# Optimization experiments

Measured on AMD Instinct MI355X. Metric: run time of the kernel, lower is better.

Reference implementation:

```python
import jax, jax.numpy as jnp
import numpy as np

EPS = 1e-05


def _inv_sqrt_22(M):
    # M: [C, 2, 2] SPD. Closed-form sqrt via trace/det, then analytic 2x2 inverse.
    a, b = M[:, 0, 0], M[:, 0, 1]
    c, d = M[:, 1, 0], M[:, 1, 1]
    s = jnp.sqrt(a * d - b * c)            # sqrt(det)
    t = jnp.sqrt(a + d + 2.0 * s)          # sqrt(trace + 2*sqrt(det))
    # M_sqrt = (M + s*I)/t ; invert analytically
    sa, sb, sc, sd = (a + s) / t, b / t, c / t, (d + s) / t
    det_sqrt = sa * sd - sb * sc
    inv = jnp.stack([jnp.stack([sd, -sb], -1), jnp.stack([-sc, sa], -1)], -2)
    return inv / det_sqrt[:, None, None]   # [C, 2, 2]


def setup_inputs() -> dict:
    key = jax.random.key(0)
    k1, k2, k3 = jax.random.split(key, 3)
    B, C, H, W = 32, 64, 128, 128
    z = jax.random.normal(k1, (B, C, H, W, 2), dtype=jnp.float32)
    gamma = jax.random.normal(k2, (2, 2), dtype=jnp.float32)
    beta = jax.random.normal(k3, (2,), dtype=jnp.float32)
    return {"z": z, "gamma": gamma, "beta": beta}


def reference(z, gamma, beta):
    # z: [B, C, H, W, 2] real view of a complex feature map (training-mode path)
    B, C, H, W, _ = z.shape
    mu = jnp.mean(z, axis=(0, 2, 3), keepdims=True)          # [1,C,1,1,2]
    xc = z - mu
    # per-channel 2x2 covariance
    sigma = jnp.einsum('bchwi,bchwj->cij', xc, xc) / (B * H * W)
    sigma = sigma + EPS * jnp.eye(2, dtype=z.dtype)
    w = _inv_sqrt_22(sigma)                                   # [C,2,2]
    o = jnp.einsum('cij,bchwj->bchwi', w, xc)                 # whiten
    o = jnp.einsum('ij,bchwj->bchwi', gamma, o) + beta        # affine
    return o
```

## Files before the change

kernel.cpp:

```cpp
#include <hip/hip_runtime.h>
#include <math.h>

#define EPS 1e-5

constexpr int B = 32, C = 64, H = 128, W = 128;
constexpr int HW = H * W;
constexpr int NSAMP = B * HW;
constexpr int PLANE_FLOATS = HW * 2;
constexpr int PLANE_F4 = PLANE_FLOATS / 4;
constexpr int PLANES = B * C;

typedef float vfloat4 __attribute__((ext_vector_type(4)));

__global__ __launch_bounds__(256) void reduce_kernel(const float* __restrict__ z,
                                                     float* __restrict__ ws) {
    const int blk = blockIdx.x;
    const vfloat4* p = (const vfloat4*)(z + (size_t)blk * PLANE_FLOATS);

    float s0 = 0.f, s1 = 0.f, s00 = 0.f, s01 = 0.f, s11 = 0.f;
    for (int base = 0; base < PLANE_F4; base += 1024) {
        const int i = base + threadIdx.x;
        vfloat4 v0 = p[i];
        vfloat4 v1 = p[i + 256];
        vfloat4 v2 = p[i + 512];
        vfloat4 v3 = p[i + 768];
        s0  += (v0.x + v0.z) + (v1.x + v1.z) + (v2.x + v2.z) + (v3.x + v3.z);
        s1  += (v0.y + v0.w) + (v1.y + v1.w) + (v2.y + v2.w) + (v3.y + v3.w);
        s00 += (v0.x * v0.x + v0.z * v0.z) + (v1.x * v1.x + v1.z * v1.z)
             + (v2.x * v2.x + v2.z * v2.z) + (v3.x * v3.x + v3.z * v3.z);
        s11 += (v0.y * v0.y + v0.w * v0.w) + (v1.y * v1.y + v1.w * v1.w)
             + (v2.y * v2.y + v2.w * v2.w) + (v3.y * v3.y + v3.w * v3.w);
        s01 += (v0.x * v0.y + v0.z * v0.w) + (v1.x * v1.y + v1.z * v1.w)
             + (v2.x * v2.y + v2.z * v2.w) + (v3.x * v3.y + v3.z * v3.w);
    }

    #pragma unroll
    for (int o = 32; o > 0; o >>= 1) {
        s0  += __shfl_down(s0,  o, 64);
        s1  += __shfl_down(s1,  o, 64);
        s00 += __shfl_down(s00, o, 64);
        s01 += __shfl_down(s01, o, 64);
        s11 += __shfl_down(s11, o, 64);
    }

    __shared__ float sm[5][4];
    const int lane = threadIdx.x & 63;
    const int wv = threadIdx.x >> 6;
    if (lane == 0) {
        sm[0][wv] = s0; sm[1][wv] = s1; sm[2][wv] = s00; sm[3][wv] = s01; sm[4][wv] = s11;
    }
    __syncthreads();
    if (threadIdx.x == 0) {
        float t0 = 0.f, t1 = 0.f, t2 = 0.f, t3 = 0.f, t4 = 0.f;
        #pragma unroll
        for (int w = 0; w < 4; w++) {
            t0 += sm[0][w]; t1 += sm[1][w]; t2 += sm[2][w]; t3 += sm[3][w]; t4 += sm[4][w];
        }
        float* wp = ws + (size_t)blk * 8;
        wp[0] = t0; wp[1] = t1; wp[2] = t2; wp[3] = t3; wp[4] = t4;
    }
}

__global__ __launch_bounds__(256) void apply_kernel(const float* __restrict__ z,
                                                    const float* __restrict__ ws,
                                                    const float* __restrict__ gamma,
                                                    const float* __restrict__ beta,
                                                    float* __restrict__ out) {
    const int blk = blockIdx.x;
    const int c = blk & (C - 1);

    __shared__ float tr[6];
    if (threadIdx.x < 64) {
        float a0 = 0.f, a1 = 0.f, a2 = 0.f, a3 = 0.f, a4 = 0.f;
        if (threadIdx.x < B) {
            const float* wp = ws + (size_t)(threadIdx.x * C + c) * 8;
            a0 = wp[0]; a1 = wp[1]; a2 = wp[2]; a3 = wp[3]; a4 = wp[4];
        }
        #pragma unroll
        for (int o = 16; o > 0; o >>= 1) {
            a0 += __shfl_down(a0, o, 64);
            a1 += __shfl_down(a1, o, 64);
            a2 += __shfl_down(a2, o, 64);
            a3 += __shfl_down(a3, o, 64);
            a4 += __shfl_down(a4, o, 64);
        }
        if (threadIdx.x == 0) {
            const double S0 = a0, S1 = a1, S00 = a2, S01 = a3, S11 = a4;
            const double invN = 1.0 / (double)NSAMP;
            const double mu0 = S0 * invN, mu1 = S1 * invN;
            const double va = S00 * invN - mu0 * mu0 + EPS;
            const double vb = S01 * invN - mu0 * mu1;
            const double vd = S11 * invN - mu1 * mu1 + EPS;
            const double sdet = sqrt(va * vd - vb * vb);
            const double tt = sqrt(va + vd + 2.0 * sdet);
            const double sa = (va + sdet) / tt;
            const double sb = vb / tt;
            const double sd2 = (vd + sdet) / tt;
            const double inv_det = 1.0 / (sa * sd2 - sb * sb);
            const double w00 =  sd2 * inv_det;
            const double w01 = -sb  * inv_det;
            const double w11 =  sa  * inv_det;
            const double g00 = gamma[0], g01 = gamma[1], g10 = gamma[2], g11 = gamma[3];
            const double A00 = g00 * w00 + g01 * w01;
            const double A01 = g00 * w01 + g01 * w11;
            const double A10 = g10 * w00 + g11 * w01;
            const double A11 = g10 * w01 + g11 * w11;
            tr[0] = (float)A00; tr[1] = (float)A01; tr[2] = (float)A10; tr[3] = (float)A11;
            tr[4] = (float)((double)beta[0] - (A00 * mu0 + A01 * mu1));
            tr[5] = (float)((double)beta[1] - (A10 * mu0 + A11 * mu1));
        }
    }
    __syncthreads();
    const float A00 = tr[0], A01 = tr[1], A10 = tr[2], A11 = tr[3];
    const float b0 = tr[4], b1 = tr[5];

    const vfloat4* p = (const vfloat4*)(z + (size_t)blk * PLANE_FLOATS);
    vfloat4* q = (vfloat4*)(out + (size_t)blk * PLANE_FLOATS);
    for (int base = PLANE_F4 - 1024; base >= 0; base -= 1024) {
        const int i = base + threadIdx.x;
        vfloat4 v0 = p[i];
        vfloat4 v1 = p[i + 256];
        vfloat4 v2 = p[i + 512];
        vfloat4 v3 = p[i + 768];
        vfloat4 r0, r1, r2, r3;
        r0.x = A00 * v0.x + A01 * v0.y + b0;  r0.y = A10 * v0.x + A11 * v0.y + b1;
        r0.z = A00 * v0.z + A01 * v0.w + b0;  r0.w = A10 * v0.z + A11 * v0.w + b1;
        r1.x = A00 * v1.x + A01 * v1.y + b0;  r1.y = A10 * v1.x + A11 * v1.y + b1;
        r1.z = A00 * v1.z + A01 * v1.w + b0;  r1.w = A10 * v1.z + A11 * v1.w + b1;
        r2.x = A00 * v2.x + A01 * v2.y + b0;  r2.y = A10 * v2.x + A11 * v2.y + b1;
        r2.z = A00 * v2.z + A01 * v2.w + b0;  r2.w = A10 * v2.z + A11 * v2.w + b1;
        r3.x = A00 * v3.x + A01 * v3.y + b0;  r3.y = A10 * v3.x + A11 * v3.y + b1;
        r3.z = A00 * v3.z + A01 * v3.w + b0;  r3.w = A10 * v3.z + A11 * v3.w + b1;
        __builtin_nontemporal_store(r0, &q[i]);
        __builtin_nontemporal_store(r1, &q[i + 256]);
        __builtin_nontemporal_store(r2, &q[i + 512]);
        __builtin_nontemporal_store(r3, &q[i + 768]);
    }
}

extern "C" void kernel_launch(void* const* d_in, const int* in_sizes, int n_in,
                              void* d_out, int out_size, void* d_ws, size_t ws_size,
                              hipStream_t stream) {
    (void)in_sizes; (void)n_in; (void)out_size; (void)ws_size;
    const float* z     = (const float*)d_in[0];
    const float* gamma = (const float*)d_in[1];
    const float* beta  = (const float*)d_in[2];
    float* out = (float*)d_out;
    float* ws  = (float*)d_ws;

    reduce_kernel<<<PLANES, 256, 0, stream>>>(z, ws);
    apply_kernel<<<PLANES, 256, 0, stream>>>(z, ws, gamma, beta, out);
}
```

Baseline: 476.8 us.

## Fuse reduce and apply into one persistent kernel with per-channel flag sync

Replaces the two-kernel reduce/apply scheme with one kernel of 256 blocks of 1024 threads, each owning a quarter of the batch for one channel. Blocks publish partial sums, bump a per-channel atomic counter and spin until all four quarters arrive, then build the affine transform and apply it, re-reading their planes in reverse order to hit in cache. The aim is to remove one launch and reuse cached input between the reduce and apply phases. The risks are a deadlock if the blocks are not all co-resident, lower parallelism from fewer blocks, and an extra memset launch.

```diff
diff --git a/kernel.cpp b/kernel.cpp
--- a/kernel.cpp
+++ b/kernel.cpp
@@ -8,30 +8,50 @@
 constexpr int NSAMP = B * HW;
 constexpr int PLANE_FLOATS = HW * 2;
 constexpr int PLANE_F4 = PLANE_FLOATS / 4;
-constexpr int PLANES = B * C;
+constexpr int QUARTERS = 4;
+constexpr int PLANES_PER_BLK = B / QUARTERS;
+constexpr int NBLOCKS = C * QUARTERS;
+constexpr int NTHREADS = 1024;
 
 typedef float vfloat4 __attribute__((ext_vector_type(4)));
 
-__global__ __launch_bounds__(256) void reduce_kernel(const float* __restrict__ z,
-                                                     float* __restrict__ ws) {
-    const int blk = blockIdx.x;
-    const vfloat4* p = (const vfloat4*)(z + (size_t)blk * PLANE_FLOATS);
+__device__ __forceinline__ float agent_load_f32(const float* a) {
+    unsigned int u = __hip_atomic_load((const unsigned int*)a,
+                                       __ATOMIC_RELAXED, __HIP_MEMORY_SCOPE_AGENT);
+    return __uint_as_float(u);
+}
+
+__global__ __launch_bounds__(NTHREADS) void fused_kernel(
+    const float* __restrict__ z, float* __restrict__ ws,
+    const float* __restrict__ gamma, const float* __restrict__ beta,
+    float* __restrict__ out)
+{
+    const int k = blockIdx.x;
+    const int c = k & (C - 1);
+    const int q = k >> 6;
+    int* flags = (int*)ws;
+    float* part = ws + 64;
 
     float s0 = 0.f, s1 = 0.f, s00 = 0.f, s01 = 0.f, s11 = 0.f;
-    for (int base = 0; base < PLANE_F4; base += 1024) {
-        const int i = base + threadIdx.x;
-        vfloat4 v0 = p[i];
-        vfloat4 v1 = p[i + 256];
-        vfloat4 v2 = p[i + 512];
-        vfloat4 v3 = p[i + 768];
-        s0  += (v0.x + v0.z) + (v1.x + v1.z) + (v2.x + v2.z) + (v3.x + v3.z);
-        s1  += (v0.y + v0.w) + (v1.y + v1.w) + (v2.y + v2.w) + (v3.y + v3.w);
-        s00 += (v0.x * v0.x + v0.z * v0.z) + (v1.x * v1.x + v1.z * v1.z)
-             + (v2.x * v2.x + v2.z * v2.z) + (v3.x * v3.x + v3.z * v3.z);
-        s11 += (v0.y * v0.y + v0.w * v0.w) + (v1.y * v1.y + v1.w * v1.w)
-             + (v2.y * v2.y + v2.w * v2.w) + (v3.y * v3.y + v3.w * v3.w);
-        s01 += (v0.x * v0.y + v0.z * v0.w) + (v1.x * v1.y + v1.z * v1.w)
-             + (v2.x * v2.y + v2.z * v2.w) + (v3.x * v3.y + v3.z * v3.w);
+    for (int j = 0; j < PLANES_PER_BLK; ++j) {
+        const int plane = (q * PLANES_PER_BLK + j) * C + c;
+        const vfloat4* p = (const vfloat4*)(z + (size_t)plane * PLANE_FLOATS);
+        #pragma unroll
+        for (int base = 0; base < PLANE_F4; base += 4096) {
+            const int i = base + threadIdx.x;
+            vfloat4 v0 = p[i];
+            vfloat4 v1 = p[i + 1024];
+            vfloat4 v2 = p[i + 2048];
+            vfloat4 v3 = p[i + 3072];
+            s0  += (v0.x + v0.z) + (v1.x + v1.z) + (v2.x + v2.z) + (v3.x + v3.z);
+            s1  += (v0.y + v0.w) + (v1.y + v1.w) + (v2.y + v2.w) + (v3.y + v3.w);
+            s00 += (v0.x * v0.x + v0.z * v0.z) + (v1.x * v1.x + v1.z * v1.z)
+                 + (v2.x * v2.x + v2.z * v2.z) + (v3.x * v3.x + v3.z * v3.z);
+            s11 += (v0.y * v0.y + v0.w * v0.w) + (v1.y * v1.y + v1.w * v1.w)
+                 + (v2.y * v2.y + v2.w * v2.w) + (v3.y * v3.y + v3.w * v3.w);
+            s01 += (v0.x * v0.y + v0.z * v0.w) + (v1.x * v1.y + v1.z * v1.w)
+                 + (v2.x * v2.y + v2.z * v2.w) + (v3.x * v3.y + v3.z * v3.w);
+        }
     }
 
     #pragma unroll
@@ -43,98 +63,94 @@
         s11 += __shfl_down(s11, o, 64);
     }
 
-    __shared__ float sm[5][4];
+    __shared__ float sm[5][16];
     const int lane = threadIdx.x & 63;
     const int wv = threadIdx.x >> 6;
     if (lane == 0) {
         sm[0][wv] = s0; sm[1][wv] = s1; sm[2][wv] = s00; sm[3][wv] = s01; sm[4][wv] = s11;
     }
     __syncthreads();
+
+    __shared__ float tr[6];
     if (threadIdx.x == 0) {
         float t0 = 0.f, t1 = 0.f, t2 = 0.f, t3 = 0.f, t4 = 0.f;
         #pragma unroll
-        for (int w = 0; w < 4; w++) {
+        for (int w = 0; w < 16; w++) {
             t0 += sm[0][w]; t1 += sm[1][w]; t2 += sm[2][w]; t3 += sm[3][w]; t4 += sm[4][w];
         }
-        float* wp = ws + (size_t)blk * 8;
+        float* wp = part + (size_t)k * 8;
         wp[0] = t0; wp[1] = t1; wp[2] = t2; wp[3] = t3; wp[4] = t4;
-    }
-}
+        __threadfence();
+        atomicAdd(&flags[c], 1);
 
-__global__ __launch_bounds__(256) void apply_kernel(const float* __restrict__ z,
-                                                    const float* __restrict__ ws,
-                                                    const float* __restrict__ gamma,
-                                                    const float* __restrict__ beta,
-                                                    float* __restrict__ out) {
-    const int blk = blockIdx.x;
-    const int c = blk & (C - 1);
+        while (__hip_atomic_load(&flags[c], __ATOMIC_ACQUIRE,
+                                 __HIP_MEMORY_SCOPE_AGENT) < QUARTERS) {
+            __builtin_amdgcn_s_sleep(8);
+        }
 
-    __shared__ float tr[6];
-    if (threadIdx.x < 64) {
-        float a0 = 0.f, a1 = 0.f, a2 = 0.f, a3 = 0.f, a4 = 0.f;
-        if (threadIdx.x < B) {
-            const float* wp = ws + (size_t)(threadIdx.x * C + c) * 8;
-            a0 = wp[0]; a1 = wp[1]; a2 = wp[2]; a3 = wp[3]; a4 = wp[4];
+        double S0 = 0.0, S1 = 0.0, S00 = 0.0, S01 = 0.0, S11 = 0.0;
+        #pragma unroll
+        for (int qq = 0; qq < QUARTERS; ++qq) {
+            const float* pp = part + (size_t)(qq * C + c) * 8;
+            S0  += (double)agent_load_f32(pp + 0);
+            S1  += (double)agent_load_f32(pp + 1);
+            S00 += (double)agent_load_f32(pp + 2);
+            S01 += (double)agent_load_f32(pp + 3);
+            S11 += (double)agent_load_f32(pp + 4);
         }
-        #pragma unroll
-        for (int o = 16; o > 0; o >>= 1) {
-            a0 += __shfl_down(a0, o, 64);
-            a1 += __shfl_down(a1, o, 64);
-            a2 += __shfl_down(a2, o, 64);
-            a3 += __shfl_down(a3, o, 64);
-            a4 += __shfl_down(a4, o, 64);
-        }
-        if (threadIdx.x == 0) {
-            const double S0 = a0, S1 = a1, S00 = a2, S01 = a3, S11 = a4;
-            const double invN = 1.0 / (double)NSAMP;
-            const double mu0 = S0 * invN, mu1 = S1 * invN;
-            const double va = S00 * invN - mu0 * mu0 + EPS;
-            const double vb = S01 * invN - mu0 * mu1;
-            const double vd = S11 * invN - mu1 * mu1 + EPS;
-            const double sdet = sqrt(va * vd - vb * vb);
-            const double tt = sqrt(va + vd + 2.0 * sdet);
-            const double sa = (va + sdet) / tt;
-            const double sb = vb / tt;
-            const double sd2 = (vd + sdet) / tt;
-            const double inv_det = 1.0 / (sa * sd2 - sb * sb);
-            const double w00 =  sd2 * inv_det;
-            const double w01 = -sb  * inv_det;
-            const double w11 =  sa  * inv_det;
-            const double g00 = gamma[0], g01 = gamma[1], g10 = gamma[2], g11 = gamma[3];
-            const double A00 = g00 * w00 + g01 * w01;
-            const double A01 = g00 * w01 + g01 * w11;
-            const double A10 = g10 * w00 + g11 * w01;
-            const double A11 = g10 * w01 + g11 * w11;
-            tr[0] = (float)A00; tr[1] = (float)A01; tr[2] = (float)A10; tr[3] = (float)A11;
-            tr[4] = (float)((double)beta[0] - (A00 * mu0 + A01 * mu1));
-            tr[5] = (float)((double)beta[1] - (A10 * mu0 + A11 * mu1));
-        }
+        const double invN = 1.0 / (double)NSAMP;
+        const double mu0 = S0 * invN, mu1 = S1 * invN;
+        const double va = S00 * invN - mu0 * mu0 + EPS;
+        const double vb = S01 * invN - mu0 * mu1;
+        const double vd = S11 * invN - mu1 * mu1 + EPS;
+        const double sdet = sqrt(va * vd - vb * vb);
+        const double tt = sqrt(va + vd + 2.0 * sdet);
+        const double sa = (va + sdet) / tt;
+        const double sb = vb / tt;
+        const double sd2 = (vd + sdet) / tt;
+        const double inv_det = 1.0 / (sa * sd2 - sb * sb);
+        const double w00 =  sd2 * inv_det;
+        const double w01 = -sb  * inv_det;
+        const double w11 =  sa  * inv_det;
+        const double g00 = gamma[0], g01 = gamma[1], g10 = gamma[2], g11 = gamma[3];
+        const double A00 = g00 * w00 + g01 * w01;
+        const double A01 = g00 * w01 + g01 * w11;
+        const double A10 = g10 * w00 + g11 * w01;
+        const double A11 = g10 * w01 + g11 * w11;
+        tr[0] = (float)A00; tr[1] = (float)A01; tr[2] = (float)A10; tr[3] = (float)A11;
+        tr[4] = (float)((double)beta[0] - (A00 * mu0 + A01 * mu1));
+        tr[5] = (float)((double)beta[1] - (A10 * mu0 + A11 * mu1));
     }
     __syncthreads();
     const float A00 = tr[0], A01 = tr[1], A10 = tr[2], A11 = tr[3];
     const float b0 = tr[4], b1 = tr[5];
 
-    const vfloat4* p = (const vfloat4*)(z + (size_t)blk * PLANE_FLOATS);
-    vfloat4* q = (vfloat4*)(out + (size_t)blk * PLANE_FLOATS);
-    for (int base = PLANE_F4 - 1024; base >= 0; base -= 1024) {
-        const int i = base + threadIdx.x;
-        vfloat4 v0 = p[i];
-        vfloat4 v1 = p[i + 256];
-        vfloat4 v2 = p[i + 512];
-        vfloat4 v3 = p[i + 768];
-        vfloat4 r0, r1, r2, r3;
-        r0.x = A00 * v0.x + A01 * v0.y + b0;  r0.y = A10 * v0.x + A11 * v0.y + b1;
-        r0.z = A00 * v0.z + A01 * v0.w + b0;  r0.w = A10 * v0.z + A11 * v0.w + b1;
-        r1.x = A00 * v1.x + A01 * v1.y + b0;  r1.y = A10 * v1.x + A11 * v1.y + b1;
-        r1.z = A00 * v1.z + A01 * v1.w + b0;  r1.w = A10 * v1.z + A11 * v1.w + b1;
-        r2.x = A00 * v2.x + A01 * v2.y + b0;  r2.y = A10 * v2.x + A11 * v2.y + b1;
-        r2.z = A00 * v2.z + A01 * v2.w + b0;  r2.w = A10 * v2.z + A11 * v2.w + b1;
-        r3.x = A00 * v3.x + A01 * v3.y + b0;  r3.y = A10 * v3.x + A11 * v3.y + b1;
-        r3.z = A00 * v3.z + A01 * v3.w + b0;  r3.w = A10 * v3.z + A11 * v3.w + b1;
-        __builtin_nontemporal_store(r0, &q[i]);
-        __builtin_nontemporal_store(r1, &q[i + 256]);
-        __builtin_nontemporal_store(r2, &q[i + 512]);
-        __builtin_nontemporal_store(r3, &q[i + 768]);
+    for (int j = PLANES_PER_BLK - 1; j >= 0; --j) {
+        const int plane = (q * PLANES_PER_BLK + j) * C + c;
+        const size_t off = (size_t)plane * PLANE_FLOATS;
+        const vfloat4* p = (const vfloat4*)(z + off);
+        vfloat4* qo = (vfloat4*)(out + off);
+        #pragma unroll
+        for (int base = PLANE_F4 - 4096; base >= 0; base -= 4096) {
+            const int i = base + threadIdx.x;
+            vfloat4 v0 = p[i];
+            vfloat4 v1 = p[i + 1024];
+            vfloat4 v2 = p[i + 2048];
+            vfloat4 v3 = p[i + 3072];
+            vfloat4 r0, r1, r2, r3;
+            r0.x = A00 * v0.x + A01 * v0.y + b0;  r0.y = A10 * v0.x + A11 * v0.y + b1;
+            r0.z = A00 * v0.z + A01 * v0.w + b0;  r0.w = A10 * v0.z + A11 * v0.w + b1;
+            r1.x = A00 * v1.x + A01 * v1.y + b0;  r1.y = A10 * v1.x + A11 * v1.y + b1;
+            r1.z = A00 * v1.z + A01 * v1.w + b0;  r1.w = A10 * v1.z + A11 * v1.w + b1;
+            r2.x = A00 * v2.x + A01 * v2.y + b0;  r2.y = A10 * v2.x + A11 * v2.y + b1;
+            r2.z = A00 * v2.z + A01 * v2.w + b0;  r2.w = A10 * v2.z + A11 * v2.w + b1;
+            r3.x = A00 * v3.x + A01 * v3.y + b0;  r3.y = A10 * v3.x + A11 * v3.y + b1;
+            r3.z = A00 * v3.z + A01 * v3.w + b0;  r3.w = A10 * v3.z + A11 * v3.w + b1;
+            __builtin_nontemporal_store(r0, &qo[i]);
+            __builtin_nontemporal_store(r1, &qo[i + 1024]);
+            __builtin_nontemporal_store(r2, &qo[i + 2048]);
+            __builtin_nontemporal_store(r3, &qo[i + 3072]);
+        }
     }
 }
 
@@ -148,6 +164,6 @@
     float* out = (float*)d_out;
     float* ws  = (float*)d_ws;
 
-    reduce_kernel<<<PLANES, 256, 0, stream>>>(z, ws);
-    apply_kernel<<<PLANES, 256, 0, stream>>>(z, ws, gamma, beta, out);
+    (void)hipMemsetAsync(ws, 0, C * sizeof(int), stream);
+    fused_kernel<<<NBLOCKS, NTHREADS, 0, stream>>>(z, ws, gamma, beta, out);
 }
```

After: 479.7 us. No clear change (+0.6%).

## Fuse reduce and apply kernels with per-channel atomic spin barrier

Applied to the files above, without the earlier changes.

Merges the statistics reduction and the whitening/affine pass into one kernel. Each block publishes its partial sums, increments a per-channel counter and spins until all batch slices of that channel have arrived, then reads the partials with agent-scope loads. The aim is to drop the second kernel launch and let the re-read of the plane hit in cache shortly after the first read. It relies on every block in the grid being co-resident, enforced only by a launch bound of 8 blocks per CU. If that does not hold, it deadlocks. A memset of the flags is added before the launch.

```diff
diff --git a/kernel.cpp b/kernel.cpp
--- a/kernel.cpp
+++ b/kernel.cpp
@@ -9,14 +9,27 @@
 constexpr int PLANE_FLOATS = HW * 2;
 constexpr int PLANE_F4 = PLANE_FLOATS / 4;
 constexpr int PLANES = B * C;
+constexpr int NTHREADS = 256;
 
 typedef float vfloat4 __attribute__((ext_vector_type(4)));
 
-__global__ __launch_bounds__(256) void reduce_kernel(const float* __restrict__ z,
-                                                     float* __restrict__ ws) {
-    const int blk = blockIdx.x;
-    const vfloat4* p = (const vfloat4*)(z + (size_t)blk * PLANE_FLOATS);
+__device__ __forceinline__ float agent_load_f32(const float* a) {
+    unsigned int u = __hip_atomic_load((const unsigned int*)a,
+                                       __ATOMIC_RELAXED, __HIP_MEMORY_SCOPE_AGENT);
+    return __uint_as_float(u);
+}
 
+__global__ __launch_bounds__(NTHREADS, 8) void fused_kernel(
+    const float* __restrict__ z, float* __restrict__ ws,
+    const float* __restrict__ gamma, const float* __restrict__ beta,
+    float* __restrict__ out)
+{
+    const int k = blockIdx.x;
+    const int c = k & (C - 1);
+    int* flags = (int*)ws;
+    float* part = ws + 64;
+
+    const vfloat4* p = (const vfloat4*)(z + (size_t)k * PLANE_FLOATS);
     float s0 = 0.f, s1 = 0.f, s00 = 0.f, s01 = 0.f, s11 = 0.f;
     for (int base = 0; base < PLANE_F4; base += 1024) {
         const int i = base + threadIdx.x;
@@ -50,31 +63,34 @@
         sm[0][wv] = s0; sm[1][wv] = s1; sm[2][wv] = s00; sm[3][wv] = s01; sm[4][wv] = s11;
     }
     __syncthreads();
+
     if (threadIdx.x == 0) {
         float t0 = 0.f, t1 = 0.f, t2 = 0.f, t3 = 0.f, t4 = 0.f;
         #pragma unroll
         for (int w = 0; w < 4; w++) {
             t0 += sm[0][w]; t1 += sm[1][w]; t2 += sm[2][w]; t3 += sm[3][w]; t4 += sm[4][w];
         }
-        float* wp = ws + (size_t)blk * 8;
+        float* wp = part + (size_t)k * 8;
         wp[0] = t0; wp[1] = t1; wp[2] = t2; wp[3] = t3; wp[4] = t4;
+        __threadfence();
+        atomicAdd(&flags[c], 1);
+        while (__hip_atomic_load(&flags[c], __ATOMIC_ACQUIRE,
+                                 __HIP_MEMORY_SCOPE_AGENT) < B) {
+            __builtin_amdgcn_s_sleep(2);
+        }
     }
-}
-
-__global__ __launch_bounds__(256) void apply_kernel(const float* __restrict__ z,
-                                                    const float* __restrict__ ws,
-                                                    const float* __restrict__ gamma,
-                                                    const float* __restrict__ beta,
-                                                    float* __restrict__ out) {
-    const int blk = blockIdx.x;
-    const int c = blk & (C - 1);
+    __syncthreads();
 
     __shared__ float tr[6];
     if (threadIdx.x < 64) {
         float a0 = 0.f, a1 = 0.f, a2 = 0.f, a3 = 0.f, a4 = 0.f;
         if (threadIdx.x < B) {
-            const float* wp = ws + (size_t)(threadIdx.x * C + c) * 8;
-            a0 = wp[0]; a1 = wp[1]; a2 = wp[2]; a3 = wp[3]; a4 = wp[4];
+            const float* pp = part + (size_t)(threadIdx.x * C + c) * 8;
+            a0 = agent_load_f32(pp + 0);
+            a1 = agent_load_f32(pp + 1);
+            a2 = agent_load_f32(pp + 2);
+            a3 = agent_load_f32(pp + 3);
+            a4 = agent_load_f32(pp + 4);
         }
         #pragma unroll
         for (int o = 16; o > 0; o >>= 1) {
@@ -114,8 +130,7 @@
     const float A00 = tr[0], A01 = tr[1], A10 = tr[2], A11 = tr[3];
     const float b0 = tr[4], b1 = tr[5];
 
-    const vfloat4* p = (const vfloat4*)(z + (size_t)blk * PLANE_FLOATS);
-    vfloat4* q = (vfloat4*)(out + (size_t)blk * PLANE_FLOATS);
+    vfloat4* qo = (vfloat4*)(out + (size_t)k * PLANE_FLOATS);
     for (int base = PLANE_F4 - 1024; base >= 0; base -= 1024) {
         const int i = base + threadIdx.x;
         vfloat4 v0 = p[i];
@@ -131,10 +146,10 @@
         r2.z = A00 * v2.z + A01 * v2.w + b0;  r2.w = A10 * v2.z + A11 * v2.w + b1;
         r3.x = A00 * v3.x + A01 * v3.y + b0;  r3.y = A10 * v3.x + A11 * v3.y + b1;
         r3.z = A00 * v3.z + A01 * v3.w + b0;  r3.w = A10 * v3.z + A11 * v3.w + b1;
-        __builtin_nontemporal_store(r0, &q[i]);
-        __builtin_nontemporal_store(r1, &q[i + 256]);
-        __builtin_nontemporal_store(r2, &q[i + 512]);
-        __builtin_nontemporal_store(r3, &q[i + 768]);
+        __builtin_nontemporal_store(r0, &qo[i]);
+        __builtin_nontemporal_store(r1, &qo[i + 256]);
+        __builtin_nontemporal_store(r2, &qo[i + 512]);
+        __builtin_nontemporal_store(r3, &qo[i + 768]);
     }
 }
 
@@ -148,6 +163,6 @@
     float* out = (float*)d_out;
     float* ws  = (float*)d_ws;
 
-    reduce_kernel<<<PLANES, 256, 0, stream>>>(z, ws);
-    apply_kernel<<<PLANES, 256, 0, stream>>>(z, ws, gamma, beta, out);
+    (void)hipMemsetAsync(ws, 0, C * sizeof(int), stream);
+    fused_kernel<<<PLANES, NTHREADS, 0, stream>>>(z, ws, gamma, beta, out);
 }
```

Result: slower. 733.1 us (+53.7%).
